# Optimization experiments

Hardware: AMD Instinct MI355X
Metric: run time of the kernel (lower is better)

Reference implementation:

```python
import jax, jax.numpy as jnp
import numpy as np

B = 2
T = 32768          # exp.n_samples = 2**15
NB = 128           # exp.n_bands (filter bank bands)
CH = 128           # channels
EC = 512           # encoding_channels
ATOM = 2048        # full_atom_size
FBK = 512          # filter bank kernel size
DILS = (1, 3, 9, 27, 81, 243, 1)


def setup_inputs() -> dict:
    key = jax.random.key(0)
    ks = jax.random.split(key, 8)
    s = 0.05
    return {
        'x': jax.random.normal(ks[0], (B, 1, T), jnp.float32),
        'fb_w': jax.random.normal(ks[1], (NB, 1, FBK), jnp.float32) * s,
        'conv0_w': jax.random.normal(ks[2], (CH, NB, 7), jnp.float32) * s,
        'conv0_b': jnp.zeros((CH,), jnp.float32),
        'bn0_g': jnp.ones((CH,), jnp.float32),
        'bn0_b': jnp.zeros((CH,), jnp.float32),
        'dil_w': jax.random.normal(ks[3], (7, CH, CH, 3), jnp.float32) * s,
        'dil_b': jnp.zeros((7, CH), jnp.float32),
        'pw_w': jax.random.normal(ks[4], (7, CH, CH, 1), jnp.float32) * s,
        'pw_b': jnp.zeros((7, CH), jnp.float32),
        'bn_g': jnp.ones((7, CH), jnp.float32),
        'bn_b': jnp.zeros((7, CH), jnp.float32),
        'up_w': jax.random.normal(ks[5], (EC, CH, 1), jnp.float32) * s,
        'up_b': jnp.zeros((EC,), jnp.float32),
        'static_dict': jax.random.uniform(ks[6], (1, EC, ATOM), jnp.float32, -1.0, 1.0),
    }


def _conv1d(x, w, b=None, dilation=1, padding=0):
    y = jax.lax.conv_general_dilated(
        x, w, (1,), [(padding, padding)], rhs_dilation=(dilation,),
        dimension_numbers=('NCH', 'OIH', 'NCH'))
    if b is not None:
        y = y + b[None, :, None]
    return y


def _bn(x, g, b, eps=1e-5):
    # BatchNorm1d in training mode: per-channel stats over (batch, time)
    m = x.mean(axis=(0, 2), keepdims=True)
    v = x.var(axis=(0, 2), keepdims=True)
    return (x - m) * jax.lax.rsqrt(v + eps) * g[None, :, None] + b[None, :, None]


def _lrelu(x):
    return jnp.where(x >= 0, x, 0.2 * x)


def _fft_convolve(a, b):
    # linear convolution via zero-padded rfft, truncated back to n samples
    n = a.shape[-1]
    fa = jnp.fft.rfft(a, n=2 * n, axis=-1)
    fb = jnp.fft.rfft(b, n=2 * n, axis=-1)
    return jnp.fft.irfft(fa * fb, n=2 * n, axis=-1)[..., :n]


def reference(x, fb_w, conv0_w, conv0_b, bn0_g, bn0_b, dil_w, dil_b,
              pw_w, pw_b, bn_g, bn_b, up_w, up_b, static_dict):
    Bsz, _, n = x.shape
    # filter bank analysis: [B,1,T] -> [B,NB,T]
    spec = _conv1d(x, fb_w, padding=FBK // 2)[..., :n]
    # front conv + leaky relu + BN
    h = _conv1d(spec, conv0_w, conv0_b, padding=3)
    h = _bn(_lrelu(h), bn0_g, bn0_b)
    # dilated residual blocks (dropout = identity at inference)
    for i, d in enumerate(DILS):
        orig = h
        y = _conv1d(h, dil_w[i], dil_b[i], dilation=d, padding=d)
        y = _conv1d(y, pw_w[i], pw_b[i])
        h = _bn(_lrelu(y + orig), bn_g[i], bn_b[i])
    # up-projection to encoding channels + relu
    encoding = jax.nn.relu(_conv1d(h, up_w, up_b))  # [B,EC,T]
    # static dictionary atoms, zero-padded to n_samples, convolved with encoding
    atoms = jnp.broadcast_to(static_dict, (Bsz, EC, ATOM))
    atoms = jnp.pad(atoms, ((0, 0), (0, 0), (0, n - ATOM)))
    final = _fft_convolve(atoms, encoding)          # [B,EC,T]
    return jnp.sum(final, axis=1, keepdims=True)    # [B,1,T]
```

## Files before the change

### kernel.cpp

```cpp
#include <hip/hip_runtime.h>
#include <hip/hip_bf16.h>

#define B_ 2
#define T_ 32768
#define CH_ 128
#define EC_ 512
#define ATOM_ 2048
#define FBK_ 512

typedef __attribute__((ext_vector_type(8))) short s16x8;
typedef __attribute__((ext_vector_type(8))) _Float16 f16x8;
typedef __attribute__((ext_vector_type(4))) float f32x4;

__device__ __forceinline__ f16x8 ldh8(const _Float16* p) {
    union { s16x8 s; f16x8 h; } u; u.s = *(const s16x8*)p; return u.h;
}

__device__ __forceinline__ void gl_lds16(const _Float16* g, _Float16* l) {
    __builtin_amdgcn_global_load_lds(
        (const __attribute__((address_space(1))) unsigned int*)(g),
        (__attribute__((address_space(3))) unsigned int*)(l), 16, 0, 0);
}

__global__ void __launch_bounds__(256) k_fbm(const float* __restrict__ x,
        const _Float16* __restrict__ Wfb, _Float16* __restrict__ spec16) {
    __shared__ _Float16 XA[128][72];
    __shared__ float xw[640];
    int tid = threadIdx.x;
    int lane = tid & 63;
    int wv = tid >> 6, wm = wv >> 1, wn = wv & 1;
    int ln15 = lane & 15, kh = lane >> 4;
    int t0 = blockIdx.x * 128;
    int b = blockIdx.y;

    for (int i = tid; i < 640; i += 256) {
        int g = t0 - 256 + i;
        xw[i] = (g >= 0 && g < T_) ? x[(size_t)b*T_ + g] : 0.f;
    }

    f32x4 acc[4][4];
    f32x4 zero = {0.f,0.f,0.f,0.f};
#pragma unroll
    for (int m = 0; m < 4; ++m)
#pragma unroll
        for (int n = 0; n < 4; ++n) acc[m][n] = zero;

    for (int c = 0; c < 8; ++c) {
        int k0 = c*64;
        __syncthreads();
#pragma unroll
        for (int q = 0; q < 4; ++q) {
            int idx = tid + q*256;
            int r = idx >> 3, ko = idx & 7;
            int base = r + k0 + ko*8;
            f16x8 v;
#pragma unroll
            for (int j = 0; j < 8; ++j) v[j] = (_Float16)xw[base + j];
            union { f16x8 h; s16x8 s; } u; u.h = v;
            *(s16x8*)&XA[r][ko*8] = u.s;
        }
        __syncthreads();
#pragma unroll
        for (int kt = 0; kt < 2; ++kt) {
            f16x8 af[4], bf[4];
#pragma unroll
            for (int m = 0; m < 4; ++m) af[m] = ldh8(&XA[wm*64+m*16+ln15][kt*32+kh*8]);
#pragma unroll
            for (int n = 0; n < 4; ++n)
                bf[n] = ldh8(Wfb + (size_t)(wn*64+n*16+ln15)*FBK_ + k0 + kt*32 + kh*8);
#pragma unroll
            for (int m = 0; m < 4; ++m)
#pragma unroll
                for (int n = 0; n < 4; ++n)
                    acc[m][n] = __builtin_amdgcn_mfma_f32_16x16x32_f16(af[m], bf[n], acc[m][n], 0,0,0);
        }
    }
#pragma unroll
    for (int mf = 0; mf < 4; ++mf)
#pragma unroll
        for (int nf = 0; nf < 4; ++nf) {
            int band = wn*64 + nf*16 + ln15;
#pragma unroll
            for (int j = 0; j < 4; ++j) {
                int tl = wm*64 + mf*16 + kh*4 + j;
                spec16[((size_t)b*T_ + t0 + tl)*CH_ + band] = (_Float16)acc[mf][nf][j];
            }
        }
}

__global__ void k_pw7(const float* __restrict__ w, _Float16* __restrict__ W7) {
    int i = blockIdx.x*256+threadIdx.x;
    if (i >= 7*16384) return;
    int k = i / 16384, r = i % 16384; int co = r >> 7, ci = r & 127;
    W7[i] = (_Float16)w[(co*CH_+ci)*7 + k];
}
__global__ void k_pwd(const float* __restrict__ w, _Float16* __restrict__ Wd) {
    int i = blockIdx.x*256+threadIdx.x;
    if (i >= 7*3*16384) return;
    int st = i / 49152, r = i % 49152; int k = r / 16384, r2 = r % 16384;
    int co = r2 >> 7, ci = r2 & 127;
    Wd[i] = (_Float16)w[((size_t)(st*CH_+co)*CH_+ci)*3 + k];
}
__global__ void k_cast(const float* __restrict__ in, _Float16* __restrict__ out, int n) {
    int i = blockIdx.x*256+threadIdx.x;
    if (i < n) out[i] = (_Float16)in[i];
}
__global__ void k_zero(float* __restrict__ p, int n) {
    int i = blockIdx.x*256+threadIdx.x;
    if (i < n) p[i] = 0.f;
}

template<int NTAP, bool NORM, bool PW, bool LRELU, bool RELU, bool STATS>
__global__ void __launch_bounds__(256) k_cv(
        const _Float16* __restrict__ in, const _Float16* __restrict__ W,
        const float* __restrict__ bias, const _Float16* __restrict__ Wp_,
        const float* __restrict__ pbias, const float* __restrict__ stats_in,
        const float* __restrict__ g, const float* __restrict__ bb,
        float* __restrict__ stats_out, _Float16* __restrict__ outp,
        int dil, int ostride) {
    __shared__ _Float16 XT[128][136];
    __shared__ _Float16 Y1[PW?128:1][PW?136:1];
    __shared__ float AffA[NORM?128:1], AffB[NORM?128:1];

    int tid = threadIdx.x;
    int lane = tid & 63;
    int wv = tid >> 6, wm = wv >> 1, wn = wv & 1;
    int ln15 = lane & 15, kh = lane >> 4;
    int t0 = blockIdx.x * 128;
    int nch = blockIdx.y;
    int b = blockIdx.z;
    int ncol0 = nch * 128;
    const _Float16* inb = in + (size_t)b*T_*CH_;
    const _Float16* W_eff = W + (size_t)ncol0*CH_;
    const float* bias_eff = bias + ncol0;

    if (NORM) {
        if (tid < 128) {
            const float invN = 1.f/(float)(B_*T_);
            float s1 = stats_in[tid], s2 = stats_in[128+tid];
            float m = s1*invN, var = s2*invN - m*m;
            float A = rsqrtf(var + 1e-5f) * g[tid];
            AffA[tid] = A; AffB[tid] = bb[tid] - m*A;
        }
    }

    f32x4 acc[4][4];
    f32x4 zero = {0.f,0.f,0.f,0.f};
#pragma unroll
    for (int m = 0; m < 4; ++m)
#pragma unroll
        for (int n = 0; n < 4; ++n) acc[m][n] = zero;

    for (int tap = 0; tap < NTAP; ++tap) {
        int tp = tap;
        if (PW) tp = (tap==0) ? 0 : ((tap==1) ? 2 : 1);
        int off = (tp - NTAP/2)*dil;
        const _Float16* Wt = W_eff + (size_t)tp*CH_*CH_;
        __syncthreads();
#pragma unroll
        for (int q = 0; q < 8; ++q) {
            int idx = tid + q*256;
            int lt = idx >> 4, ck = idx & 15;
            int gt = t0 + lt + off;
            s16x8 v = {0,0,0,0,0,0,0,0};
            bool valid = (gt >= 0 && gt < T_);
            if (valid) {
                v = *(const s16x8*)(inb + (size_t)gt*CH_ + ck*8);
                if (NORM) {
                    union {s16x8 s; f16x8 h;} u; u.s = v;
                    f16x8 r;
#pragma unroll
                    for (int j = 0; j < 8; ++j) {
                        float f = (float)u.h[j];
                        f = fmaf(f, AffA[ck*8+j], AffB[ck*8+j]);
                        r[j] = (_Float16)f;
                    }
                    union {f16x8 h; s16x8 s;} w2; w2.h = r; v = w2.s;
                }
            }
            *(s16x8*)&XT[lt][ck*8] = v;
        }
        __syncthreads();
#pragma unroll
        for (int kt = 0; kt < 4; ++kt) {
            f16x8 af[4], bf[4];
#pragma unroll
            for (int m = 0; m < 4; ++m) af[m] = ldh8(&XT[wm*64+m*16+ln15][kt*32+kh*8]);
#pragma unroll
            for (int n = 0; n < 4; ++n)
                bf[n] = ldh8(Wt + (size_t)(wn*64+n*16+ln15)*CH_ + kt*32 + kh*8);
#pragma unroll
            for (int m = 0; m < 4; ++m)
#pragma unroll
                for (int n = 0; n < 4; ++n)
                    acc[m][n] = __builtin_amdgcn_mfma_f32_16x16x32_f16(af[m], bf[n], acc[m][n], 0,0,0);
        }
    }

    if (PW) {
#pragma unroll
        for (int mf = 0; mf < 4; ++mf)
#pragma unroll
            for (int nf = 0; nf < 4; ++nf) {
                int co = wn*64 + nf*16 + ln15;
                float bv = bias_eff[co];
#pragma unroll
                for (int j = 0; j < 4; ++j) {
                    int tl = wm*64 + mf*16 + kh*4 + j;
                    Y1[tl][co] = (_Float16)(acc[mf][nf][j] + bv);
                }
            }
#pragma unroll
        for (int m = 0; m < 4; ++m)
#pragma unroll
            for (int n = 0; n < 4; ++n) acc[m][n] = zero;
        __syncthreads();
#pragma unroll
        for (int kt = 0; kt < 4; ++kt) {
            f16x8 af[4], bf[4];
#pragma unroll
            for (int m = 0; m < 4; ++m) af[m] = ldh8(&Y1[wm*64+m*16+ln15][kt*32+kh*8]);
#pragma unroll
            for (int n = 0; n < 4; ++n)
                bf[n] = ldh8(Wp_ + (size_t)(wn*64+n*16+ln15)*CH_ + kt*32 + kh*8);
#pragma unroll
            for (int m = 0; m < 4; ++m)
#pragma unroll
                for (int n = 0; n < 4; ++n)
                    acc[m][n] = __builtin_amdgcn_mfma_f32_16x16x32_f16(af[m], bf[n], acc[m][n], 0,0,0);
        }
    }

#pragma unroll
    for (int nf = 0; nf < 4; ++nf) {
        int co = wn*64 + nf*16 + ln15;
        float bfin = PW ? pbias[co] : bias_eff[co];
        float s = 0.f, s2 = 0.f;
#pragma unroll
        for (int mf = 0; mf < 4; ++mf) {
#pragma unroll
            for (int j = 0; j < 4; ++j) {
                int tl = wm*64 + mf*16 + kh*4 + j;
                float v = acc[mf][nf][j] + bfin;
                if (PW) v += (float)XT[tl][co];
                if (LRELU) v = v >= 0.f ? v : 0.2f*v;
                if (RELU)  v = fmaxf(v, 0.f);
                outp[((size_t)b*T_ + t0 + tl)*ostride + ncol0 + co] = (_Float16)v;
                if (STATS) { s += v; s2 += v*v; }
            }
        }
        if (STATS) {
            s  += __shfl_down(s, 16);  s  += __shfl_down(s, 32);
            s2 += __shfl_down(s2, 16); s2 += __shfl_down(s2, 32);
            if (kh == 0) {
                atomicAdd(&stats_out[co], s);
                atomicAdd(&stats_out[128+co], s2);
            }
        }
    }
}

__global__ void k_tr_at(const float* __restrict__ sd, _Float16* __restrict__ At) {
    __shared__ float tile[32][33];
    int tau0 = blockIdx.x*32;
    int c0 = blockIdx.y*32;
    int tx = threadIdx.x, ty = threadIdx.y;
#pragma unroll
    for (int j = 0; j < 4; ++j)
        tile[ty+j*8][tx] = sd[(size_t)(c0+ty+j*8)*ATOM_ + tau0 + tx];
    __syncthreads();
#pragma unroll
    for (int j = 0; j < 4; ++j)
        At[(size_t)(tau0+ty+j*8)*EC_ + c0 + tx] = (_Float16)tile[tx][ty+j*8];
}

__global__ void __launch_bounds__(256) k_gemm(const _Float16* __restrict__ At,
                                              const _Float16* __restrict__ enc,
                                              float* __restrict__ out) {
    __shared__ _Float16 lA[128*64];
    __shared__ _Float16 lB[128*64];
    __shared__ float pt[256];
    int tid = threadIdx.x;
    int lane = tid & 63;
    int wv = tid >> 6;
    int wm = wv >> 1, wn = wv & 1;
    int tT = blockIdx.x;
    int sT = blockIdx.y;
    int b  = blockIdx.z;
    const _Float16* Ab = At + (size_t)tT*128*EC_;
    const _Float16* Eb = enc + ((size_t)b*T_ + (size_t)sT*128)*EC_;
    int ln15 = lane & 15, kh = lane >> 4;
    int lrow = lane >> 3;
    int lcol = (lane & 7)*8;
    f32x4 acc[4][4];
    f32x4 zero = {0.f,0.f,0.f,0.f};
#pragma unroll
    for (int m = 0; m < 4; ++m)
#pragma unroll
        for (int n = 0; n < 4; ++n) acc[m][n] = zero;

    for (int kt = 0; kt < 8; ++kt) {
        int k0 = kt*64;
#pragma unroll
        for (int c = 0; c < 4; ++c) {
            int brow = wv*32 + c*8;
            gl_lds16(Ab + (size_t)(brow + lrow)*EC_ + k0 + lcol, &lA[brow*64]);
            gl_lds16(Eb + (size_t)(brow + lrow)*EC_ + k0 + lcol, &lB[brow*64]);
        }
        __syncthreads();
#pragma unroll
        for (int kk = 0; kk < 2; ++kk) {
            f16x8 af[4], bfr[4];
#pragma unroll
            for (int m = 0; m < 4; ++m)
                af[m] = ldh8(&lA[(wm*64 + m*16 + ln15)*64 + kk*32 + kh*8]);
#pragma unroll
            for (int n = 0; n < 4; ++n)
                bfr[n] = ldh8(&lB[(wn*64 + n*16 + ln15)*64 + kk*32 + kh*8]);
#pragma unroll
            for (int m = 0; m < 4; ++m)
#pragma unroll
                for (int n = 0; n < 4; ++n)
                    acc[m][n] = __builtin_amdgcn_mfma_f32_16x16x32_f16(af[m], bfr[n], acc[m][n], 0, 0, 0);
        }
        __syncthreads();
    }

    pt[tid] = 0.f;
    __syncthreads();
#pragma unroll
    for (int mn = 0; mn <= 6; ++mn) {
#pragma unroll
        for (int j = 0; j < 4; ++j) {
            float v = 0.f;
#pragma unroll
            for (int m = 0; m < 4; ++m) {
                int n = mn - m;
                if (n >= 0 && n < 4) v += acc[m][n][j];
            }
            int tl = (wm + wn)*64 + mn*16 + kh*4 + j + ln15;
            unsafeAtomicAdd(&pt[tl], v);
        }
    }
    __syncthreads();
    if (tid < 255) {
        int tg = tT*128 + sT*128 + tid;
        if (tg < T_) unsafeAtomicAdd(&out[(size_t)b*T_ + tg], pt[tid]);
    }
}

__global__ void k_fill(float* __restrict__ out, float val) {
    out[blockIdx.x*256 + threadIdx.x] = val;
}

extern "C" void kernel_launch(void* const* d_in, const int* in_sizes, int n_in,
                              void* d_out, int out_size, void* d_ws, size_t ws_size,
                              hipStream_t stream) {
    const float* x       = (const float*)d_in[0];
    const float* fb_w    = (const float*)d_in[1];
    const float* conv0_w = (const float*)d_in[2];
    const float* conv0_b = (const float*)d_in[3];
    const float* bn0_g   = (const float*)d_in[4];
    const float* bn0_b   = (const float*)d_in[5];
    const float* dil_w   = (const float*)d_in[6];
    const float* dil_b   = (const float*)d_in[7];
    const float* pw_w    = (const float*)d_in[8];
    const float* pw_b    = (const float*)d_in[9];
    const float* bn_g    = (const float*)d_in[10];
    const float* bn_b    = (const float*)d_in[11];
    const float* up_w    = (const float*)d_in[12];
    const float* up_b    = (const float*)d_in[13];
    const float* sdict   = (const float*)d_in[14];
    float* out = (float*)d_out;
    char* ws = (char*)d_ws;

    const size_t R1   = 33554432;
    const size_t R2   = 33554432;
    const size_t ACT  = 16777216;
    char* r1   = ws;
    char* actA = ws + R1 + R2;
    char* actB = actA + ACT;
    char* wreg = actB + ACT;
    _Float16* W7   = (_Float16*)wreg;
    _Float16* Wd   = W7 + 7*16384;
    _Float16* Wp   = Wd + 7*3*16384;
    _Float16* Wup  = Wp + 7*16384;
    _Float16* Wfb  = Wup + 65536;
    float* stats   = (float*)(Wfb + 65536);
    const size_t TOTAL = R1 + R2 + 2*ACT
                       + (7*16384 + 7*3*16384 + 7*16384 + 65536 + 65536)*2 + 8*2*128*4;
    if (ws_size < TOTAL) {
        k_fill<<<(out_size+255)/256, 256, 0, stream>>>(out, 12345.0f);
        return;
    }
    _Float16* spec16 = (_Float16*)r1;
    _Float16* enc = (_Float16*)r1;
    _Float16* At  = (_Float16*)(actA + 2097152);

    k_zero<<<(2048+255)/256, 256, 0, stream>>>(stats, 8*2*128);
    k_pw7<<<(7*16384+255)/256, 256, 0, stream>>>(conv0_w, W7);
    k_pwd<<<(7*3*16384+255)/256, 256, 0, stream>>>(dil_w, Wd);
    k_cast<<<(7*16384+255)/256, 256, 0, stream>>>(pw_w, Wp, 7*16384);
    k_cast<<<(65536+255)/256, 256, 0, stream>>>(up_w, Wup, 65536);
    k_cast<<<(65536+255)/256, 256, 0, stream>>>(fb_w, Wfb, 65536);

    k_fbm<<<dim3(T_/128, B_), 256, 0, stream>>>(x, Wfb, spec16);
    k_cv<7,false,false,true,false,true><<<dim3(T_/128,1,B_), 256, 0, stream>>>(
        spec16, W7, conv0_b, nullptr, nullptr, nullptr, nullptr, nullptr,
        stats + 0, (_Float16*)actA, 1, CH_);

    const int DILS[7] = {1, 3, 9, 27, 81, 243, 1};
    _Float16* cur = (_Float16*)actA;
    _Float16* nxt = (_Float16*)actB;
    for (int i = 0; i < 7; ++i) {
        const float* gi = (i == 0) ? bn0_g : bn_g + (i-1)*CH_;
        const float* bi = (i == 0) ? bn0_b : bn_b + (i-1)*CH_;
        k_cv<3,true,true,true,false,true><<<dim3(T_/128,1,B_), 256, 0, stream>>>(
            cur, Wd + (size_t)i*3*CH_*CH_, dil_b + i*CH_, Wp + (size_t)i*CH_*CH_,
            pw_b + i*CH_, stats + i*256, gi, bi, stats + (i+1)*256, nxt, DILS[i], CH_);
        _Float16* sw = cur; cur = nxt; nxt = sw;
    }

    k_tr_at<<<dim3(ATOM_/32, EC_/32), dim3(32,8), 0, stream>>>(sdict, At);
    k_cv<1,true,false,false,true,false><<<dim3(T_/128,EC_/128,B_), 256, 0, stream>>>(
        cur, Wup, up_b, nullptr, nullptr,
        stats + 7*256, bn_g + 6*CH_, bn_b + 6*CH_, nullptr, enc, 1, EC_);

    k_zero<<<(B_*T_+255)/256, 256, 0, stream>>>(out, B_*T_);
    k_gemm<<<dim3(ATOM_/128, T_/128, B_), 256, 0, stream>>>(At, enc, out);
}
```

Before: 983.3 us.

## Swizzle GEMM LDS layout and remap block order for L2 reuse

Applies an XOR swizzle to the 16-byte chunk column on both the global-to-LDS loads and the fragment reads of the Toeplitz GEMM, so the row-strided fragment loads no longer land on the same LDS banks. Blocks are also remapped into groups of 4 time tiles × 16 atom tiles, so blocks running together share encoding and atom tiles in L2. The partial-sum buffer is now zeroed at kernel start, which drops one barrier before the epilogue. The change is mainly about fewer LDS bank conflicts and better cache locality. Correctness depends on the swizzle matching between the writes and the reads.

```diff
diff --git a/kernel.cpp b/kernel.cpp
--- a/kernel.cpp
+++ b/kernel.cpp
@@ -284,14 +284,18 @@
     int lane = tid & 63;
     int wv = tid >> 6;
     int wm = wv >> 1, wn = wv & 1;
-    int tT = blockIdx.x;
-    int sT = blockIdx.y;
-    int b  = blockIdx.z;
+    int id = blockIdx.x;
+    int sOuter = id >> 6;
+    int inner  = id & 63;
+    int tT = inner >> 2;
+    int sT = sOuter*4 + (inner & 3);
+    int b  = blockIdx.y;
     const _Float16* Ab = At + (size_t)tT*128*EC_;
     const _Float16* Eb = enc + ((size_t)b*T_ + (size_t)sT*128)*EC_;
     int ln15 = lane & 15, kh = lane >> 4;
     int lrow = lane >> 3;
-    int lcol = (lane & 7)*8;
+    int scol = (((lane & 7) ^ lrow)) * 8;
+    pt[tid] = 0.f;
     f32x4 acc[4][4];
     f32x4 zero = {0.f,0.f,0.f,0.f};
 #pragma unroll
@@ -304,19 +308,23 @@
 #pragma unroll
         for (int c = 0; c < 4; ++c) {
             int brow = wv*32 + c*8;
-            gl_lds16(Ab + (size_t)(brow + lrow)*EC_ + k0 + lcol, &lA[brow*64]);
-            gl_lds16(Eb + (size_t)(brow + lrow)*EC_ + k0 + lcol, &lB[brow*64]);
+            gl_lds16(Ab + (size_t)(brow + lrow)*EC_ + k0 + scol, &lA[brow*64]);
+            gl_lds16(Eb + (size_t)(brow + lrow)*EC_ + k0 + scol, &lB[brow*64]);
         }
         __syncthreads();
 #pragma unroll
         for (int kk = 0; kk < 2; ++kk) {
             f16x8 af[4], bfr[4];
 #pragma unroll
-            for (int m = 0; m < 4; ++m)
-                af[m] = ldh8(&lA[(wm*64 + m*16 + ln15)*64 + kk*32 + kh*8]);
-#pragma unroll
-            for (int n = 0; n < 4; ++n)
-                bfr[n] = ldh8(&lB[(wn*64 + n*16 + ln15)*64 + kk*32 + kh*8]);
+            for (int m = 0; m < 4; ++m) {
+                int r = wm*64 + m*16 + ln15;
+                af[m] = ldh8(&lA[r*64 + (((kk<<2)|kh) ^ (r & 7))*8]);
+            }
+#pragma unroll
+            for (int n = 0; n < 4; ++n) {
+                int r = wn*64 + n*16 + ln15;
+                bfr[n] = ldh8(&lB[r*64 + (((kk<<2)|kh) ^ (r & 7))*8]);
+            }
 #pragma unroll
             for (int m = 0; m < 4; ++m)
 #pragma unroll
@@ -326,8 +334,6 @@
         __syncthreads();
     }
 
-    pt[tid] = 0.f;
-    __syncthreads();
 #pragma unroll
     for (int mn = 0; mn <= 6; ++mn) {
 #pragma unroll
@@ -427,5 +433,5 @@
         stats + 7*256, bn_g + 6*CH_, bn_b + 6*CH_, nullptr, enc, 1, EC_);
 
     k_zero<<<(B_*T_+255)/256, 256, 0, stream>>>(out, B_*T_);
-    k_gemm<<<dim3(ATOM_/128, T_/128, B_), 256, 0, stream>>>(At, enc, out);
-}
+    k_gemm<<<dim3(4096, B_), 256, 0, stream>>>(At, enc, out);
+}
```

Result: faster. 941.3 us (-4.3%).
